# Kernel optimization log

Hardware: AMD Instinct MI355X
Metric: run time of the kernel (lower is better)

Reference implementation:

```python
import jax, jax.numpy as jnp
import numpy as np


def setup_inputs() -> dict:
    key = jax.random.key(0)
    k1, k2 = jax.random.split(key)
    B, Fin, N = 8, 64, 4096
    Fout, K = 64, 20
    x = jax.random.normal(k1, (B, Fin, N), dtype=jnp.float32)
    W = jax.random.normal(k2, (Fout, 2 * Fin), dtype=jnp.float32) * (1.0 / np.sqrt(2 * Fin))
    b = jnp.zeros((Fout,), dtype=jnp.float32)
    return {"x": x, "W": W, "b": b, "k": K}


def reference(x, W, b, k):
    # x: [B, Fin, N]; W: [Fout, 2Fin] (1x1 conv weight); b: [Fout]
    B, Fin, N = x.shape
    xt = jnp.swapaxes(x, 1, 2)                      # [B, N, Fin]
    sq = jnp.sum(xt * xt, axis=2)                   # [B, N]
    # pairwise squared distances: ||xi||^2 - 2 xi.xj + ||xj||^2
    dist = -2.0 * jnp.einsum('bnf,bmf->bnm', xt, xt) + sq[:, :, None] + sq[:, None, :]
    # ascending sort, drop self (index 0), keep k nearest neighbors
    idx = jnp.argsort(dist, axis=2)[:, :, 1:k + 1]  # [B, N, k] int
    # gather neighbor features per batch
    nbr = jax.vmap(lambda pts, i: pts[i])(xt, idx)  # [B, N, k, Fin]
    central = xt[:, :, None, :]                     # [B, N, 1, Fin]
    ee = jnp.concatenate(
        [jnp.broadcast_to(central, (B, N, k, Fin)), nbr - central], axis=-1
    )                                               # [B, N, k, 2Fin]
    # 1x1 conv == dense over channel dim, then bias, then max over k
    h = jnp.einsum('bnkf,of->bnko', ee, W) + b      # [B, N, k, Fout]
    out = jnp.max(h, axis=2)                        # [B, N, Fout]
    return jnp.swapaxes(out, 1, 2)                  # [B, Fout, N]
```

## Files before the change

kernel.cpp:

```cpp
#include <hip/hip_runtime.h>
#include <hip/hip_bf16.h>
#include <float.h>


#define BB 8
#define FF 64
#define NN 4096
#define KK 20
#define CAP 64
#define SS 2
#define PAD 0.3f

typedef unsigned short ushort_t;
typedef unsigned long long u64;
typedef __attribute__((ext_vector_type(8))) _Float16 half8;
typedef __attribute__((ext_vector_type(4))) float floatx4;
typedef __attribute__((ext_vector_type(2))) float floatx2;
typedef __attribute__((ext_vector_type(2))) unsigned short ushortx2;
typedef __attribute__((ext_vector_type(4))) unsigned int uintx4;

__device__ __forceinline__ size_t plidx16(int b, int n, int k) {
  return ((size_t)b * 256 + (n >> 4)) * 1024 + (size_t)(k >> 3) * 128 + (size_t)(n & 15) * 8 + (k & 7);
}

__global__ void __launch_bounds__(256) prep_kernel(
    const float* __restrict__ x, const float* __restrict__ W,
    float* __restrict__ sq, float* __restrict__ Q,
    ushort_t* __restrict__ ph, ushort_t* __restrict__ pm)
{
  __shared__ float xs[64][65];
  __shared__ float w2[64][65];
  int t = threadIdx.x;
  int b = blockIdx.x >> 6;
  int n0 = (blockIdx.x & 63) << 6;
  const float* xb = x + (size_t)b * FF * NN;

  int nl = t & 63, fq = t >> 6;
  #pragma unroll
  for (int i = 0; i < 16; ++i) {
    int f = fq + i * 4;
    xs[f][nl] = xb[(size_t)f * NN + n0 + nl];
  }
  #pragma unroll
  for (int i = 0; i < 16; ++i) {
    int id = i * 256 + t;
    int o = id >> 6, f = id & 63;
    w2[o][f] = W[o * 128 + 64 + f];
  }
  __syncthreads();

  if (t < 64) {
    float s = 0.f;
    #pragma unroll
    for (int f = 0; f < FF; ++f) { float v = xs[f][t]; s += v * v; }
    sq[b * NN + n0 + t] = s;
  }
  int o = t & 63, g = t >> 6;
  for (int i = 0; i < 16; ++i) {
    int r = g + i * 4;
    int n = n0 + r;
    float acc = 0.f;
    #pragma unroll
    for (int f = 0; f < FF; ++f) acc += w2[o][f] * xs[f][r];
    Q[((size_t)b * NN + n) * FF + o] = acc;

    float v = xs[o][r] * 1.41421356237309515f;
    _Float16 hh = (_Float16)v;
    float hf = (float)hh;
    _Float16 mm = (_Float16)((v - hf) * 4096.0f);
    size_t pb = plidx16(b, n, o);
    ph[pb] = __builtin_bit_cast(unsigned short, hh);
    pm[pb] = __builtin_bit_cast(unsigned short, mm);
  }
}

__device__ __forceinline__ void bitonic32f(float& v0, float& v1, int l15)
{
  #pragma unroll
  for (int k = 2; k <= 32; k <<= 1) {
    #pragma unroll
    for (int j = k >> 1; j >= 1; j >>= 1) {
      bool dirup = ((2 * l15) & k) == 0;
      if (j >= 2) {
        int lj = j >> 1;
        float p0 = __shfl_xor(v0, lj, 16);
        float p1 = __shfl_xor(v1, lj, 16);
        bool lower = (l15 & lj) == 0;
        bool keepmin = (dirup == lower);
        v0 = keepmin ? fminf(v0, p0) : fmaxf(v0, p0);
        v1 = keepmin ? fminf(v1, p1) : fmaxf(v1, p1);
      } else {
        float lo = fminf(v0, v1), hi = fmaxf(v0, v1);
        v0 = dirup ? lo : hi;
        v1 = dirup ? hi : lo;
      }
    }
  }
}

__device__ __forceinline__ void bitonic64k(u64& v0, u64& v1, int l31)
{
  #pragma unroll
  for (int k = 2; k <= 64; k <<= 1) {
    #pragma unroll
    for (int j = k >> 1; j >= 1; j >>= 1) {
      bool dirup = ((2 * l31) & k) == 0;
      if (j >= 2) {
        int lj = j >> 1;
        u64 p0 = __shfl_xor(v0, lj, 32);
        u64 p1 = __shfl_xor(v1, lj, 32);
        bool lower = (l31 & lj) == 0;
        bool keepmin = (dirup == lower);
        u64 a0 = v0 < p0 ? v0 : p0, b0 = v0 < p0 ? p0 : v0;
        u64 a1 = v1 < p1 ? v1 : p1, b1 = v1 < p1 ? p1 : v1;
        v0 = keepmin ? a0 : b0;
        v1 = keepmin ? a1 : b1;
      } else {
        u64 lo = v0 < v1 ? v0 : v1, hi = v0 < v1 ? v1 : v0;
        v0 = dirup ? lo : hi;
        v1 = dirup ? hi : lo;
      }
    }
  }
}

__device__ __forceinline__ u64 mkkey(float d, unsigned short idx)
{
  unsigned ub = __float_as_uint(d);
  unsigned mono = ub ^ (0x80000000u | (unsigned)((int)ub >> 31));
  return ((u64)mono << 16) | idx;
}

__global__ void __launch_bounds__(256) knn_kernel(
    const ushort_t* __restrict__ ph, const ushort_t* __restrict__ pm,
    const float* __restrict__ sq, u64* __restrict__ keys2)
{
  __shared__ float    bufd[4][16][CAP];
  __shared__ ushort_t bufi[4][16][CAP];
  __shared__ int scnt[4][16];

  const int t = threadIdx.x;
  const int lane = t & 63;
  const int l15 = lane & 15;
  const int q = lane >> 4;
  const int wv = t >> 6;
  const int blk = blockIdx.x;
  const int slice = blk & 1;
  const int g = (blk >> 1) & 63;
  const int b = blk >> 7;
  const int n0w = (g * 4 + wv) * 16;

  const float* __restrict__ sqb = sq + (size_t)b * NN;
  const float MS = 2.44140625e-4f;
  const int laneoff = q * 128 + l15 * 8;

  const bool hasdiag = ((n0w >> 11) == slice);
  const int dmc = (n0w & 2047) >> 5;

  half8 Ah[2], Am[2];
  {
    size_t abase = ((size_t)b * 256 + (n0w >> 4)) * 1024 + laneoff;
    #pragma unroll
    for (int s = 0; s < 2; ++s) {
      Ah[s] = *(const half8*)(ph + abase + s * 512);
      Am[s] = *(const half8*)(pm + abase + s * 512);
      uintx4 uh = __builtin_bit_cast(uintx4, Ah[s]); uh ^= 0x80008000u;
      uintx4 um = __builtin_bit_cast(uintx4, Am[s]); um ^= 0x80008000u;
      Ah[s] = __builtin_bit_cast(half8, uh);
      Am[s] = __builtin_bit_cast(half8, um);
    }
  }

  const size_t slbase = (size_t)b * 262144 + (size_t)slice * 131072 + laneoff;

  float m1[4], m2[4];
  #pragma unroll
  for (int r = 0; r < 4; ++r) { m1[r] = FLT_MAX; m2[r] = FLT_MAX; }

  {
    const ushort_t* pB = ph + slbase;
    const float* psq = sqb + slice * 2048 + l15;
    for (int mc = 0; mc < 64; ++mc) {
      float sv0 = psq[0];
      float sv1 = psq[16];
      floatx4 a1[2];
      #pragma unroll
      for (int e = 0; e < 4; ++e) { a1[0][e] = sv0; a1[1][e] = sv1; }
      #pragma unroll
      for (int ti = 0; ti < 2; ++ti) {
        #pragma unroll
        for (int s = 0; s < 2; ++s) {
          half8 Bh = *(const half8*)(pB + ti * 1024 + s * 512);
          a1[ti] = __builtin_amdgcn_mfma_f32_16x16x32_f16(Ah[s], Bh, a1[ti], 0, 0, 0);
        }
      }
      if (hasdiag && mc == dmc) {
        const int m0 = slice * 2048 + mc * 32;
        #pragma unroll
        for (int ti = 0; ti < 2; ++ti) {
          int mcol = m0 + 16 * ti + l15;
          #pragma unroll
          for (int r = 0; r < 4; ++r)
            if (mcol == n0w + 4 * q + r) a1[ti][r] = FLT_MAX;
        }
      }
      #pragma unroll
      for (int r = 0; r < 4; ++r) {
        float c = fminf(a1[0][r], a1[1][r]);
        m2[r] = __builtin_amdgcn_fmed3f(c, m1[r], m2[r]);
        m1[r] = fminf(m1[r], c);
      }
      pB += 2048;
      psq += 32;
    }
  }

  float taupad[4];
  #pragma unroll
  for (int r = 0; r < 4; ++r) {
    float v0 = m1[r], v1 = m2[r];
    bitonic32f(v0, v1, l15);
    taupad[r] = __shfl(v1, 9, 16) + PAD;
  }

  int cnt[4];
  #pragma unroll
  for (int r = 0; r < 4; ++r) cnt[r] = 0;

  {
    const ushort_t* pB = ph + slbase;
    const ushort_t* pM = pm + slbase;
    const float* psq = sqb + slice * 2048 + l15;
    for (int mc = 0; mc < 64; ++mc) {
      float sv0 = psq[0];
      float sv1 = psq[16];
      floatx4 a1[2], a2[2];
      #pragma unroll
      for (int e = 0; e < 4; ++e) {
        a1[0][e] = sv0; a1[1][e] = sv1;
        a2[0][e] = 0.f; a2[1][e] = 0.f;
      }
      #pragma unroll
      for (int ti = 0; ti < 2; ++ti) {
        #pragma unroll
        for (int s = 0; s < 2; ++s) {
          half8 Bh = *(const half8*)(pB + ti * 1024 + s * 512);
          half8 Bm = *(const half8*)(pM + ti * 1024 + s * 512);
          a1[ti] = __builtin_amdgcn_mfma_f32_16x16x32_f16(Ah[s], Bh, a1[ti], 0, 0, 0);
          a2[ti] = __builtin_amdgcn_mfma_f32_16x16x32_f16(Am[s], Bh, a2[ti], 0, 0, 0);
          a2[ti] = __builtin_amdgcn_mfma_f32_16x16x32_f16(Ah[s], Bm, a2[ti], 0, 0, 0);
        }
      }
      #pragma unroll
      for (int ti = 0; ti < 2; ++ti)
        #pragma unroll
        for (int r = 0; r < 4; ++r)
          a1[ti][r] = __builtin_fmaf(MS, a2[ti][r], a1[ti][r]);
      const int m0 = slice * 2048 + mc * 32;
      if (hasdiag && mc == dmc) {
        #pragma unroll
        for (int ti = 0; ti < 2; ++ti) {
          int mcol = m0 + 16 * ti + l15;
          #pragma unroll
          for (int r = 0; r < 4; ++r)
            if (mcol == n0w + 4 * q + r) a1[ti][r] = FLT_MAX;
        }
      }
      #pragma unroll
      for (int ti = 0; ti < 2; ++ti) {
        int mcol = m0 + 16 * ti + l15;
        #pragma unroll
        for (int r = 0; r < 4; ++r) {
          bool ok = a1[ti][r] <= taupad[r];
          unsigned long long bal = __ballot(ok);
          if (bal) {
            unsigned mh = (unsigned)((bal >> (q * 16)) & 0xFFFFull);
            int pre = __popc(mh & ((1u << l15) - 1u));
            int slot = cnt[r] + pre;
            if (ok && slot < CAP) {
              bufd[wv][4 * q + r][slot] = a1[ti][r];
              bufi[wv][4 * q + r][slot] = (ushort_t)mcol;
            }
            cnt[r] += __popc(mh);
          }
        }
      }
      pB += 2048;
      pM += 2048;
      psq += 32;
    }
  }

  if (l15 == 0) {
    #pragma unroll
    for (int r = 0; r < 4; ++r) scnt[wv][4 * q + r] = cnt[r];
  }
  __builtin_amdgcn_s_waitcnt(0);

  const int l31 = t & 31;
  const int hfw = (t >> 5) & 1;
  #pragma unroll
  for (int i = 0; i < 8; ++i) {
    int rloc = hfw * 8 + i;
    int c = scnt[wv][rloc];
    c = c < CAP ? c : CAP;
    floatx2  dv = *(const floatx2*)&bufd[wv][rloc][2 * l31];
    ushortx2 iv = *(const ushortx2*)&bufi[wv][rloc][2 * l31];
    u64 k0 = (2 * l31     < c) ? mkkey(dv[0], iv[0]) : ~0ull;
    u64 k1 = (2 * l31 + 1 < c) ? mkkey(dv[1], iv[1]) : ~0ull;
    bitonic64k(k0, k1, l31);
    u64 a = __shfl(k0, l31 >> 1, 32);
    u64 b2 = __shfl(k1, l31 >> 1, 32);
    u64 kv = (l31 & 1) ? b2 : a;
    if (l31 < KK) {
      size_t rowg = ((size_t)b * NN + n0w + rloc) * SS + slice;
      keys2[rowg * KK + l31] = kv;
    }
  }
}

__global__ void __launch_bounds__(256) merge_kernel(
    const u64* __restrict__ keys2, int* __restrict__ idxOut)
{
  int row = blockIdx.x * 256 + threadIdx.x;
  if (row >= BB * NN) return;
  u64 h[SS]; int p[SS];
  #pragma unroll
  for (int s = 0; s < SS; ++s) {
    p[s] = 0;
    h[s] = keys2[((size_t)row * SS + s) * KK];
  }
  int* op = idxOut + (size_t)row * KK;
  #pragma unroll
  for (int q = 0; q < KK; ++q) {
    int bs = 0;
    u64 bv = h[0];
    #pragma unroll
    for (int s = 1; s < SS; ++s) { if (h[s] < bv) { bv = h[s]; bs = s; } }
    op[q] = (int)(bv & 0xFFFFull);
    p[bs]++;
    h[bs] = (p[bs] < KK) ? keys2[((size_t)row * SS + bs) * KK + p[bs]] : ~0ull;
  }
}

__global__ void __launch_bounds__(256) gather_kernel(
    const float* __restrict__ x, const float* __restrict__ W,
    const float* __restrict__ bias,
    const float* __restrict__ Q, const int* __restrict__ idxIn,
    float* __restrict__ out)
{
  __shared__ float xs[64][65];
  __shared__ float wp[64][65];
  __shared__ float ot[64][65];
  __shared__ float bs[64];
  int t = threadIdx.x;
  int b = blockIdx.x >> 6;
  int n0 = (blockIdx.x & 63) << 6;
  const float* xb = x + (size_t)b * FF * NN;

  int nl0 = t & 63, fq = t >> 6;
  #pragma unroll
  for (int i = 0; i < 16; ++i) {
    int f = fq + i * 4;
    xs[f][nl0] = xb[(size_t)f * NN + n0 + nl0];
  }
  #pragma unroll
  for (int i = 0; i < 16; ++i) {
    int id = i * 256 + t;
    int o = id >> 6, f = id & 63;
    wp[o][f] = W[o * 128 + f] - W[o * 128 + 64 + f];
  }
  if (t < 64) bs[t] = bias[t];
  __syncthreads();

  int o = t & 63, g = t >> 6;
  for (int i = 0; i < 16; ++i) {
    int nl = g + i * 4;
    int n = n0 + nl;
    float p = bs[o];
    #pragma unroll
    for (int f = 0; f < FF; ++f) p += wp[o][f] * xs[f][nl];
    const int* ip = idxIn + ((size_t)b * NN + n) * KK;
    float m = -FLT_MAX;
    #pragma unroll
    for (int j = 0; j < KK; ++j) {
      int nb = ip[j];
      m = fmaxf(m, Q[((size_t)b * NN + nb) * FF + o]);
    }
    ot[nl][o] = p + m;
  }
  __syncthreads();
  for (int i = 0; i < 16; ++i) {
    int o2 = g + i * 4;
    int nl = t & 63;
    out[((size_t)b * FF + o2) * NN + n0 + nl] = ot[nl][o2];
  }
}

extern "C" void kernel_launch(void* const* d_in, const int* in_sizes, int n_in,
                              void* d_out, int out_size, void* d_ws, size_t ws_size,
                              hipStream_t stream)
{
  const float* x    = (const float*)d_in[0];
  const float* W    = (const float*)d_in[1];
  const float* bias = (const float*)d_in[2];
  float* out = (float*)d_out;

  int*   idxb = (int*)d_ws;
  float* sq   = (float*)(idxb + (size_t)BB * NN * KK);
  float* Q    = sq + (size_t)BB * NN;
  ushort_t* ph = (ushort_t*)(Q + (size_t)BB * NN * FF);
  ushort_t* pm = ph + (size_t)BB * NN * FF;
  u64*   keys2 = (u64*)(pm + (size_t)BB * NN * FF);

  prep_kernel<<<BB * (NN / 64), 256, 0, stream>>>(x, W, sq, Q, ph, pm);
  knn_kernel<<<BB * 64 * SS, 256, 0, stream>>>(ph, pm, sq, keys2);
  merge_kernel<<<(BB * NN + 255) / 256, 256, 0, stream>>>(keys2, idxb);
  gather_kernel<<<BB * (NN / 64), 256, 0, stream>>>(x, W, bias, Q, idxb, out);
}
```

Measured before the change: 263.7 us.

## Stage B tiles through double-buffered LDS and reorder block-to-batch mapping

Both kNN passes now load each 32-column B tile of the fp16 point data cooperatively into a double-buffered shared-memory stage. The next tile is prefetched from global memory while MFMAs run on the current one, with a block barrier each iteration. Before this, each wave read its B fragments straight from global memory. The block index mapping now puts batch in the low bits, and CAP shrinks to 60 to make room for the staging buffers in LDS. The added barriers and LDS traffic may offset the gain from fewer redundant global loads, and the smaller CAP raises the risk of dropping true neighbours from candidate overflow.

```diff
diff --git a/kernel.cpp b/kernel.cpp
--- a/kernel.cpp
+++ b/kernel.cpp
@@ -7,7 +7,7 @@
 #define FF 64
 #define NN 4096
 #define KK 20
-#define CAP 64
+#define CAP 60
 #define SS 2
 #define PAD 0.3f
 
@@ -135,6 +135,7 @@
     const ushort_t* __restrict__ ph, const ushort_t* __restrict__ pm,
     const float* __restrict__ sq, u64* __restrict__ keys2)
 {
+  __shared__ ushort_t stg[2][2][2048];
   __shared__ float    bufd[4][16][CAP];
   __shared__ ushort_t bufi[4][16][CAP];
   __shared__ int scnt[4][16];
@@ -145,9 +146,10 @@
   const int q = lane >> 4;
   const int wv = t >> 6;
   const int blk = blockIdx.x;
-  const int slice = blk & 1;
-  const int g = (blk >> 1) & 63;
-  const int b = blk >> 7;
+  const int b = blk & 7;
+  const int k2 = blk >> 3;
+  const int slice = k2 & 1;
+  const int g = k2 >> 1;
   const int n0w = (g * 4 + wv) * 16;
 
   const float* __restrict__ sqb = sq + (size_t)b * NN;
@@ -171,26 +173,35 @@
     }
   }
 
-  const size_t slbase = (size_t)b * 262144 + (size_t)slice * 131072 + laneoff;
+  const size_t slb = (size_t)b * 262144 + (size_t)slice * 131072;
+  const uintx4* gph = (const uintx4*)(ph + slb) + t;
+  const uintx4* gpm = (const uintx4*)(pm + slb) + t;
 
   float m1[4], m2[4];
   #pragma unroll
   for (int r = 0; r < 4; ++r) { m1[r] = FLT_MAX; m2[r] = FLT_MAX; }
 
   {
-    const ushort_t* pB = ph + slbase;
+    uintx4 v0s = gph[0];
+    *((uintx4*)stg[0][0] + t) = v0s;
+    __syncthreads();
+
     const float* psq = sqb + slice * 2048 + l15;
     for (int mc = 0; mc < 64; ++mc) {
+      const int cur = mc & 1;
+      uintx4 nx;
+      if (mc < 63) nx = gph[(mc + 1) * 256];
       float sv0 = psq[0];
       float sv1 = psq[16];
       floatx4 a1[2];
       #pragma unroll
       for (int e = 0; e < 4; ++e) { a1[0][e] = sv0; a1[1][e] = sv1; }
+      const ushort_t* sp = stg[cur][0] + laneoff;
       #pragma unroll
       for (int ti = 0; ti < 2; ++ti) {
         #pragma unroll
         for (int s = 0; s < 2; ++s) {
-          half8 Bh = *(const half8*)(pB + ti * 1024 + s * 512);
+          half8 Bh = *(const half8*)(sp + ti * 1024 + s * 512);
           a1[ti] = __builtin_amdgcn_mfma_f32_16x16x32_f16(Ah[s], Bh, a1[ti], 0, 0, 0);
         }
       }
@@ -210,7 +221,8 @@
         m2[r] = __builtin_amdgcn_fmed3f(c, m1[r], m2[r]);
         m1[r] = fminf(m1[r], c);
       }
-      pB += 2048;
+      if (mc < 63) *((uintx4*)stg[cur ^ 1][0] + t) = nx;
+      __syncthreads();
       psq += 32;
     }
   }
@@ -228,10 +240,17 @@
   for (int r = 0; r < 4; ++r) cnt[r] = 0;
 
   {
-    const ushort_t* pB = ph + slbase;
-    const ushort_t* pM = pm + slbase;
+    uintx4 vh0 = gph[0];
+    uintx4 vm0 = gpm[0];
+    *((uintx4*)stg[0][0] + t) = vh0;
+    *((uintx4*)stg[0][1] + t) = vm0;
+    __syncthreads();
+
     const float* psq = sqb + slice * 2048 + l15;
     for (int mc = 0; mc < 64; ++mc) {
+      const int cur = mc & 1;
+      uintx4 nh, nm;
+      if (mc < 63) { nh = gph[(mc + 1) * 256]; nm = gpm[(mc + 1) * 256]; }
       float sv0 = psq[0];
       float sv1 = psq[16];
       floatx4 a1[2], a2[2];
@@ -240,12 +259,14 @@
         a1[0][e] = sv0; a1[1][e] = sv1;
         a2[0][e] = 0.f; a2[1][e] = 0.f;
       }
+      const ushort_t* sp0 = stg[cur][0] + laneoff;
+      const ushort_t* sp1 = stg[cur][1] + laneoff;
       #pragma unroll
       for (int ti = 0; ti < 2; ++ti) {
         #pragma unroll
         for (int s = 0; s < 2; ++s) {
-          half8 Bh = *(const half8*)(pB + ti * 1024 + s * 512);
-          half8 Bm = *(const half8*)(pM + ti * 1024 + s * 512);
+          half8 Bh = *(const half8*)(sp0 + ti * 1024 + s * 512);
+          half8 Bm = *(const half8*)(sp1 + ti * 1024 + s * 512);
           a1[ti] = __builtin_amdgcn_mfma_f32_16x16x32_f16(Ah[s], Bh, a1[ti], 0, 0, 0);
           a2[ti] = __builtin_amdgcn_mfma_f32_16x16x32_f16(Am[s], Bh, a2[ti], 0, 0, 0);
           a2[ti] = __builtin_amdgcn_mfma_f32_16x16x32_f16(Ah[s], Bm, a2[ti], 0, 0, 0);
@@ -285,8 +306,11 @@
           }
         }
       }
-      pB += 2048;
-      pM += 2048;
+      if (mc < 63) {
+        *((uintx4*)stg[cur ^ 1][0] + t) = nh;
+        *((uintx4*)stg[cur ^ 1][1] + t) = nm;
+      }
+      __syncthreads();
       psq += 32;
     }
   }
@@ -304,10 +328,13 @@
     int rloc = hfw * 8 + i;
     int c = scnt[wv][rloc];
     c = c < CAP ? c : CAP;
-    floatx2  dv = *(const floatx2*)&bufd[wv][rloc][2 * l31];
-    ushortx2 iv = *(const ushortx2*)&bufi[wv][rloc][2 * l31];
-    u64 k0 = (2 * l31     < c) ? mkkey(dv[0], iv[0]) : ~0ull;
-    u64 k1 = (2 * l31 + 1 < c) ? mkkey(dv[1], iv[1]) : ~0ull;
+    u64 k0 = ~0ull, k1 = ~0ull;
+    if (2 * l31 < c) {
+      floatx2  dv = *(const floatx2*)&bufd[wv][rloc][2 * l31];
+      ushortx2 iv = *(const ushortx2*)&bufi[wv][rloc][2 * l31];
+      k0 = mkkey(dv[0], iv[0]);
+      if (2 * l31 + 1 < c) k1 = mkkey(dv[1], iv[1]);
+    }
     bitonic64k(k0, k1, l31);
     u64 a = __shfl(k0, l31 >> 1, 32);
     u64 b2 = __shfl(k1, l31 >> 1, 32);
```

After: 256.8 us, median of 2. 1.03x faster.

## Software-pipeline kNN B-tile loads and reorder block-to-batch mapping

Applied to the files above, without the earlier changes.

Both distance passes in the kNN kernel are unrolled by two and double-buffered in registers, so the global loads for the next column chunk are issued before the MFMA work on the current chunk, hiding load latency. The block index now takes the batch from its low bits, so adjacent blocks work on different batches. The final LDS read of candidate buffers is skipped for empty slots. More live registers could lower occupancy, and the interleaved block order may change cache locality.

```diff
diff --git a/kernel.cpp b/kernel.cpp
--- a/kernel.cpp
+++ b/kernel.cpp
@@ -145,9 +145,10 @@
   const int q = lane >> 4;
   const int wv = t >> 6;
   const int blk = blockIdx.x;
-  const int slice = blk & 1;
-  const int g = (blk >> 1) & 63;
-  const int b = blk >> 7;
+  const int b = blk & 7;
+  const int k2 = blk >> 3;
+  const int slice = k2 & 1;
+  const int g = k2 >> 1;
   const int n0w = (g * 4 + wv) * 16;
 
   const float* __restrict__ sqb = sq + (size_t)b * NN;
@@ -171,47 +172,63 @@
     }
   }
 
-  const size_t slbase = (size_t)b * 262144 + (size_t)slice * 131072 + laneoff;
+  const size_t slb = (size_t)b * 262144 + (size_t)slice * 131072 + laneoff;
 
   float m1[4], m2[4];
   #pragma unroll
   for (int r = 0; r < 4; ++r) { m1[r] = FLT_MAX; m2[r] = FLT_MAX; }
 
-  {
-    const ushort_t* pB = ph + slbase;
-    const float* psq = sqb + slice * 2048 + l15;
-    for (int mc = 0; mc < 64; ++mc) {
-      float sv0 = psq[0];
-      float sv1 = psq[16];
-      floatx4 a1[2];
-      #pragma unroll
-      for (int e = 0; e < 4; ++e) { a1[0][e] = sv0; a1[1][e] = sv1; }
+  auto bodyA = [&](int mc, half8 B00, half8 B01, half8 B10, half8 B11,
+                   float sv0, float sv1) {
+    floatx4 a1[2];
+    #pragma unroll
+    for (int e = 0; e < 4; ++e) { a1[0][e] = sv0; a1[1][e] = sv1; }
+    a1[0] = __builtin_amdgcn_mfma_f32_16x16x32_f16(Ah[0], B00, a1[0], 0, 0, 0);
+    a1[0] = __builtin_amdgcn_mfma_f32_16x16x32_f16(Ah[1], B01, a1[0], 0, 0, 0);
+    a1[1] = __builtin_amdgcn_mfma_f32_16x16x32_f16(Ah[0], B10, a1[1], 0, 0, 0);
+    a1[1] = __builtin_amdgcn_mfma_f32_16x16x32_f16(Ah[1], B11, a1[1], 0, 0, 0);
+    if (hasdiag && mc == dmc) {
+      const int m0 = slice * 2048 + mc * 32;
       #pragma unroll
       for (int ti = 0; ti < 2; ++ti) {
+        int mcol = m0 + 16 * ti + l15;
         #pragma unroll
-        for (int s = 0; s < 2; ++s) {
-          half8 Bh = *(const half8*)(pB + ti * 1024 + s * 512);
-          a1[ti] = __builtin_amdgcn_mfma_f32_16x16x32_f16(Ah[s], Bh, a1[ti], 0, 0, 0);
-        }
+        for (int r = 0; r < 4; ++r)
+          if (mcol == n0w + 4 * q + r) a1[ti][r] = FLT_MAX;
       }
-      if (hasdiag && mc == dmc) {
-        const int m0 = slice * 2048 + mc * 32;
-        #pragma unroll
-        for (int ti = 0; ti < 2; ++ti) {
-          int mcol = m0 + 16 * ti + l15;
-          #pragma unroll
-          for (int r = 0; r < 4; ++r)
-            if (mcol == n0w + 4 * q + r) a1[ti][r] = FLT_MAX;
-        }
-      }
-      #pragma unroll
-      for (int r = 0; r < 4; ++r) {
-        float c = fminf(a1[0][r], a1[1][r]);
-        m2[r] = __builtin_amdgcn_fmed3f(c, m1[r], m2[r]);
-        m1[r] = fminf(m1[r], c);
-      }
-      pB += 2048;
-      psq += 32;
+    }
+    #pragma unroll
+    for (int r = 0; r < 4; ++r) {
+      float c = fminf(a1[0][r], a1[1][r]);
+      m2[r] = __builtin_amdgcn_fmed3f(c, m1[r], m2[r]);
+      m1[r] = fminf(m1[r], c);
+    }
+  };
+
+  {
+    const ushort_t* pc = ph + slb;
+    const float* psq = sqb + slice * 2048 + l15;
+    half8 A00 = *(const half8*)(pc);
+    half8 A01 = *(const half8*)(pc + 512);
+    half8 A10 = *(const half8*)(pc + 1024);
+    half8 A11 = *(const half8*)(pc + 1536);
+    float as0 = psq[0], as1 = psq[16];
+    pc += 2048; psq += 32;
+    for (int mc = 0; mc < 64; mc += 2) {
+      half8 B00 = *(const half8*)(pc);
+      half8 B01 = *(const half8*)(pc + 512);
+      half8 B10 = *(const half8*)(pc + 1024);
+      half8 B11 = *(const half8*)(pc + 1536);
+      float bs0 = psq[0], bs1 = psq[16];
+      pc += 2048; psq += 32;
+      bodyA(mc, A00, A01, A10, A11, as0, as1);
+      A00 = *(const half8*)(pc);
+      A01 = *(const half8*)(pc + 512);
+      A10 = *(const half8*)(pc + 1024);
+      A11 = *(const half8*)(pc + 1536);
+      as0 = psq[0]; as1 = psq[16];
+      pc += 2048; psq += 32;
+      bodyA(mc + 1, B00, B01, B10, B11, bs0, bs1);
     }
   }
 
@@ -227,67 +244,100 @@
   #pragma unroll
   for (int r = 0; r < 4; ++r) cnt[r] = 0;
 
-  {
-    const ushort_t* pB = ph + slbase;
-    const ushort_t* pM = pm + slbase;
-    const float* psq = sqb + slice * 2048 + l15;
-    for (int mc = 0; mc < 64; ++mc) {
-      float sv0 = psq[0];
-      float sv1 = psq[16];
-      floatx4 a1[2], a2[2];
+  auto bodyB = [&](int mc, half8 H00, half8 H01, half8 H10, half8 H11,
+                   half8 M00, half8 M01, half8 M10, half8 M11,
+                   float sv0, float sv1) {
+    floatx4 a1[2], a2[2];
+    #pragma unroll
+    for (int e = 0; e < 4; ++e) {
+      a1[0][e] = sv0; a1[1][e] = sv1;
+      a2[0][e] = 0.f; a2[1][e] = 0.f;
+    }
+    a1[0] = __builtin_amdgcn_mfma_f32_16x16x32_f16(Ah[0], H00, a1[0], 0, 0, 0);
+    a1[0] = __builtin_amdgcn_mfma_f32_16x16x32_f16(Ah[1], H01, a1[0], 0, 0, 0);
+    a2[0] = __builtin_amdgcn_mfma_f32_16x16x32_f16(Am[0], H00, a2[0], 0, 0, 0);
+    a2[0] = __builtin_amdgcn_mfma_f32_16x16x32_f16(Am[1], H01, a2[0], 0, 0, 0);
+    a2[0] = __builtin_amdgcn_mfma_f32_16x16x32_f16(Ah[0], M00, a2[0], 0, 0, 0);
+    a2[0] = __builtin_amdgcn_mfma_f32_16x16x32_f16(Ah[1], M01, a2[0], 0, 0, 0);
+    a1[1] = __builtin_amdgcn_mfma_f32_16x16x32_f16(Ah[0], H10, a1[1], 0, 0, 0);
+    a1[1] = __builtin_amdgcn_mfma_f32_16x16x32_f16(Ah[1], H11, a1[1], 0, 0, 0);
+    a2[1] = __builtin_amdgcn_mfma_f32_16x16x32_f16(Am[0], H10, a2[1], 0, 0, 0);
+    a2[1] = __builtin_amdgcn_mfma_f32_16x16x32_f16(Am[1], H11, a2[1], 0, 0, 0);
+    a2[1] = __builtin_amdgcn_mfma_f32_16x16x32_f16(Ah[0], M10, a2[1], 0, 0, 0);
+    a2[1] = __builtin_amdgcn_mfma_f32_16x16x32_f16(Ah[1], M11, a2[1], 0, 0, 0);
+    #pragma unroll
+    for (int ti = 0; ti < 2; ++ti)
       #pragma unroll
-      for (int e = 0; e < 4; ++e) {
-        a1[0][e] = sv0; a1[1][e] = sv1;
-        a2[0][e] = 0.f; a2[1][e] = 0.f;
-      }
-      #pragma unroll
-      for (int ti = 0; ti < 2; ++ti) {
-        #pragma unroll
-        for (int s = 0; s < 2; ++s) {
-          half8 Bh = *(const half8*)(pB + ti * 1024 + s * 512);
-          half8 Bm = *(const half8*)(pM + ti * 1024 + s * 512);
-          a1[ti] = __builtin_amdgcn_mfma_f32_16x16x32_f16(Ah[s], Bh, a1[ti], 0, 0, 0);
-          a2[ti] = __builtin_amdgcn_mfma_f32_16x16x32_f16(Am[s], Bh, a2[ti], 0, 0, 0);
-          a2[ti] = __builtin_amdgcn_mfma_f32_16x16x32_f16(Ah[s], Bm, a2[ti], 0, 0, 0);
-        }
-      }
-      #pragma unroll
-      for (int ti = 0; ti < 2; ++ti)
-        #pragma unroll
-        for (int r = 0; r < 4; ++r)
-          a1[ti][r] = __builtin_fmaf(MS, a2[ti][r], a1[ti][r]);
-      const int m0 = slice * 2048 + mc * 32;
-      if (hasdiag && mc == dmc) {
-        #pragma unroll
-        for (int ti = 0; ti < 2; ++ti) {
-          int mcol = m0 + 16 * ti + l15;
-          #pragma unroll
-          for (int r = 0; r < 4; ++r)
-            if (mcol == n0w + 4 * q + r) a1[ti][r] = FLT_MAX;
-        }
-      }
+      for (int r = 0; r < 4; ++r)
+        a1[ti][r] = __builtin_fmaf(MS, a2[ti][r], a1[ti][r]);
+    const int m0 = slice * 2048 + mc * 32;
+    if (hasdiag && mc == dmc) {
       #pragma unroll
       for (int ti = 0; ti < 2; ++ti) {
         int mcol = m0 + 16 * ti + l15;
         #pragma unroll
-        for (int r = 0; r < 4; ++r) {
-          bool ok = a1[ti][r] <= taupad[r];
-          unsigned long long bal = __ballot(ok);
-          if (bal) {
-            unsigned mh = (unsigned)((bal >> (q * 16)) & 0xFFFFull);
-            int pre = __popc(mh & ((1u << l15) - 1u));
-            int slot = cnt[r] + pre;
-            if (ok && slot < CAP) {
-              bufd[wv][4 * q + r][slot] = a1[ti][r];
-              bufi[wv][4 * q + r][slot] = (ushort_t)mcol;
-            }
-            cnt[r] += __popc(mh);
+        for (int r = 0; r < 4; ++r)
+          if (mcol == n0w + 4 * q + r) a1[ti][r] = FLT_MAX;
+      }
+    }
+    #pragma unroll
+    for (int ti = 0; ti < 2; ++ti) {
+      int mcol = m0 + 16 * ti + l15;
+      #pragma unroll
+      for (int r = 0; r < 4; ++r) {
+        bool ok = a1[ti][r] <= taupad[r];
+        unsigned long long bal = __ballot(ok);
+        if (bal) {
+          unsigned mh = (unsigned)((bal >> (q * 16)) & 0xFFFFull);
+          int pre = __popc(mh & ((1u << l15) - 1u));
+          int slot = cnt[r] + pre;
+          if (ok && slot < CAP) {
+            bufd[wv][4 * q + r][slot] = a1[ti][r];
+            bufi[wv][4 * q + r][slot] = (ushort_t)mcol;
           }
+          cnt[r] += __popc(mh);
         }
       }
-      pB += 2048;
-      pM += 2048;
-      psq += 32;
+    }
+  };
+
+  {
+    const ushort_t* pch = ph + slb;
+    const ushort_t* pcm = pm + slb;
+    const float* psq = sqb + slice * 2048 + l15;
+    half8 AH00 = *(const half8*)(pch);
+    half8 AH01 = *(const half8*)(pch + 512);
+    half8 AH10 = *(const half8*)(pch + 1024);
+    half8 AH11 = *(const half8*)(pch + 1536);
+    half8 AM00 = *(const half8*)(pcm);
+    half8 AM01 = *(const half8*)(pcm + 512);
+    half8 AM10 = *(const half8*)(pcm + 1024);
+    half8 AM11 = *(const half8*)(pcm + 1536);
+    float as0 = psq[0], as1 = psq[16];
+    pch += 2048; pcm += 2048; psq += 32;
+    for (int mc = 0; mc < 64; mc += 2) {
+      half8 BH00 = *(const half8*)(pch);
+      half8 BH01 = *(const half8*)(pch + 512);
+      half8 BH10 = *(const half8*)(pch + 1024);
+      half8 BH11 = *(const half8*)(pch + 1536);
+      half8 BM00 = *(const half8*)(pcm);
+      half8 BM01 = *(const half8*)(pcm + 512);
+      half8 BM10 = *(const half8*)(pcm + 1024);
+      half8 BM11 = *(const half8*)(pcm + 1536);
+      float bs0 = psq[0], bs1 = psq[16];
+      pch += 2048; pcm += 2048; psq += 32;
+      bodyB(mc, AH00, AH01, AH10, AH11, AM00, AM01, AM10, AM11, as0, as1);
+      AH00 = *(const half8*)(pch);
+      AH01 = *(const half8*)(pch + 512);
+      AH10 = *(const half8*)(pch + 1024);
+      AH11 = *(const half8*)(pch + 1536);
+      AM00 = *(const half8*)(pcm);
+      AM01 = *(const half8*)(pcm + 512);
+      AM10 = *(const half8*)(pcm + 1024);
+      AM11 = *(const half8*)(pcm + 1536);
+      as0 = psq[0]; as1 = psq[16];
+      pch += 2048; pcm += 2048; psq += 32;
+      bodyB(mc + 1, BH00, BH01, BH10, BH11, BM00, BM01, BM10, BM11, bs0, bs1);
     }
   }
 
@@ -304,10 +354,13 @@
     int rloc = hfw * 8 + i;
     int c = scnt[wv][rloc];
     c = c < CAP ? c : CAP;
-    floatx2  dv = *(const floatx2*)&bufd[wv][rloc][2 * l31];
-    ushortx2 iv = *(const ushortx2*)&bufi[wv][rloc][2 * l31];
-    u64 k0 = (2 * l31     < c) ? mkkey(dv[0], iv[0]) : ~0ull;
-    u64 k1 = (2 * l31 + 1 < c) ? mkkey(dv[1], iv[1]) : ~0ull;
+    u64 k0 = ~0ull, k1 = ~0ull;
+    if (2 * l31 < c) {
+      floatx2  dv = *(const floatx2*)&bufd[wv][rloc][2 * l31];
+      ushortx2 iv = *(const ushortx2*)&bufi[wv][rloc][2 * l31];
+      k0 = mkkey(dv[0], iv[0]);
+      if (2 * l31 + 1 < c) k1 = mkkey(dv[1], iv[1]);
+    }
     bitonic64k(k0, k1, l31);
     u64 a = __shfl(k0, l31 >> 1, 32);
     u64 b2 = __shfl(k1, l31 >> 1, 32);
```

After: 273.1 us. 1.04x slower.
